# Optimization experiments

Hardware: AMD Instinct MI355X
Metric: run time of the kernel (lower is better)

## Reference

```python
import jax, jax.numpy as jnp
import numpy as np

B, T, NQ, NG = 8, 64, 900, 24
COST_CLS, COST_L1, COST_GIOU = 1.0, 5.0, 2.0
ALPHA, GAMMA = 0.25, 2.0


def _to_xyxy(b):
    cx, cy, w, h = b[..., 0], b[..., 1], b[..., 2], b[..., 3]
    return cx - w / 2, cy - h / 2, cx + w / 2, cy + h / 2


def _giou(a, b):
    # a, b: broadcastable (..., 4) boxes in cxcywh
    ax1, ay1, ax2, ay2 = _to_xyxy(a)
    bx1, by1, bx2, by2 = _to_xyxy(b)
    ix1 = jnp.maximum(ax1, bx1); iy1 = jnp.maximum(ay1, by1)
    ix2 = jnp.minimum(ax2, bx2); iy2 = jnp.minimum(ay2, by2)
    inter = jnp.clip(ix2 - ix1, 0) * jnp.clip(iy2 - iy1, 0)
    area_a = (ax2 - ax1) * (ay2 - ay1)
    area_b = (bx2 - bx1) * (by2 - by1)
    union = area_a + area_b - inter
    iou = inter / jnp.maximum(union, 1e-6)
    ex1 = jnp.minimum(ax1, bx1); ey1 = jnp.minimum(ay1, by1)
    ex2 = jnp.maximum(ax2, bx2); ey2 = jnp.maximum(ay2, by2)
    enc = (ex2 - ex1) * (ey2 - ey1)
    return iou - (enc - union) / jnp.maximum(enc, 1e-6)


def _cost(bboxes, scores, gt):
    # fully batched cost-matrix build across all B*T frames: (B,T,Nq,Ng)
    prob = jax.nn.sigmoid(scores)[..., 0]
    c_cls = -prob[..., None]
    c_l1 = jnp.abs(bboxes[:, :, :, None, :] - gt[:, :, None, :, :]).sum(-1)
    g = _giou(bboxes[:, :, :, None, :], gt[:, :, None, :, :])
    return COST_CLS * c_cls + COST_L1 * c_l1 - COST_GIOU * g


def _lsa(cost):
    # exact rectangular Hungarian (Jonker-Volgenant / e-maxx potentials).
    # cost: (n, m) with n <= m. Returns the column assigned to each row.
    n, m = cost.shape
    u = np.zeros(n + 1); v = np.zeros(m + 1)
    p = np.zeros(m + 1, dtype=np.int64)
    way = np.zeros(m + 1, dtype=np.int64)
    for i in range(1, n + 1):
        p[0] = i; j0 = 0
        minv = np.full(m + 1, np.inf)
        used = np.zeros(m + 1, dtype=bool)
        while True:
            used[j0] = True
            i0 = p[j0]
            jidx = np.nonzero(~used[1:])[0] + 1
            cur = cost[i0 - 1, jidx - 1] - u[i0] - v[jidx]
            better = cur < minv[jidx]
            minv[jidx] = np.where(better, cur, minv[jidx])
            way[jidx[better]] = j0
            k = jidx[np.argmin(minv[jidx])]
            delta = minv[k]
            u[p[used]] += delta
            v[used] -= delta
            minv[~used] -= delta
            j0 = k
            if p[j0] == 0:
                break
        while j0:
            j1 = way[j0]; p[j0] = p[j1]; j0 = j1
    col = np.zeros(n, dtype=np.int64)
    for j in range(1, m + 1):
        if p[j] > 0:
            col[p[j] - 1] = j - 1
    return col


def _match_all(bboxes, scores, gt):
    # mirrors the torch module's host-side scipy linear_sum_assignment per frame
    C = np.asarray(_cost(bboxes, scores, gt)).reshape(B * T, NQ, NG)
    match = np.stack([_lsa(C[f].T) for f in range(B * T)])  # query idx per GT
    return jnp.asarray(match.reshape(B, T, NG).astype(np.int32))


def _loss(bboxes, scores, gt, match):
    # focal classification loss over all queries
    tgt = jnp.minimum(jax.nn.one_hot(match, NQ, dtype=bboxes.dtype).sum(2), 1.0)[..., None]
    x = scores
    ce = tgt * jax.nn.softplus(-x) + (1.0 - tgt) * jax.nn.softplus(x)
    prob = jax.nn.sigmoid(x)
    pt = prob * tgt + (1.0 - prob) * (1.0 - tgt)
    fw = (ALPHA * tgt + (1.0 - ALPHA) * (1.0 - tgt)) * (1.0 - pt) ** GAMMA
    loss_cls = jnp.mean(fw * ce, axis=(2, 3))  # per-frame mean -> (B,T)
    idx = jnp.broadcast_to(match[..., None], (B, T, NG, 4))
    mp = jnp.take_along_axis(bboxes, idx, axis=2)  # (B,T,Ng,4)
    loss_l1 = jnp.mean(jnp.abs(mp - gt), axis=(2, 3))
    loss_g = jnp.mean(1.0 - _giou(mp, gt), axis=2)
    total = jnp.sum(loss_cls + 5.0 * loss_l1 + 2.0 * loss_g) / (B * T)
    return total.reshape(1)


def setup_inputs() -> dict:
    key = jax.random.key(0)
    k1, k2, k3 = jax.random.split(key, 3)
    return {
        "bboxes": jax.random.uniform(k1, (B, T, NQ, 4), dtype=jnp.float32),
        "scores": jax.random.normal(k2, (B, T, NQ, 1), dtype=jnp.float32),
        "gt_boxes": jax.random.uniform(k3, (B, T, NG, 4), dtype=jnp.float32),
    }


def reference(bboxes, scores, gt_boxes):
    match = _match_all(bboxes, scores, gt_boxes)
    return _loss(bboxes, scores, gt_boxes, match)
```

## Files before the change

kernel.cpp:

```cpp
#include <hip/hip_runtime.h>
#include <math.h>
#include <float.h>

#define NF 512
#define NQ 900
#define NG 24
#define NW 4
#define NCPL 4

#define ALPHA 0.25f

__device__ __forceinline__ unsigned monof(float f) {
    unsigned u = __float_as_uint(f);
    return (u & 0x80000000u) ? ~u : (u | 0x80000000u);
}
__device__ __forceinline__ float unmonof(unsigned m) {
    return (m & 0x80000000u) ? __uint_as_float(m ^ 0x80000000u)
                             : __uint_as_float(~m);
}

__device__ __forceinline__ float softplusf_(float x) {
    return fmaxf(x, 0.0f) + log1pf(expf(-fabsf(x)));
}

template <int CTRL, int RMASK>
__device__ __forceinline__ unsigned long long dpp_min_step(unsigned long long key) {
    const unsigned olo = (unsigned)__builtin_amdgcn_update_dpp(
        -1, (int)(unsigned)key, CTRL, RMASK, 0xf, false);
    const unsigned ohi = (unsigned)__builtin_amdgcn_update_dpp(
        -1, (int)(unsigned)(key >> 32), CTRL, RMASK, 0xf, false);
    const unsigned long long o = ((unsigned long long)ohi << 32) | olo;
    return (o < key) ? o : key;
}

__global__ __launch_bounds__(256) void fused_kernel(
        const float* __restrict__ bboxes,
        const float* __restrict__ scores,
        const float* __restrict__ gt,
        float* __restrict__ out)
{
    const int f = blockIdx.x;
    const int tid = threadIdx.x;
    const int lane = tid & 63;
    const int wid = tid >> 6;

    __shared__ float4 sgt[NG];
    __shared__ float u_[NG + 1];
    __shared__ int p[NQ + 1];
    __shared__ int way[NQ + 1];
    __shared__ unsigned long long swv[2][NW];
    __shared__ float lsum[NW];

    if (tid < NG) sgt[tid] = reinterpret_cast<const float4*>(gt + (size_t)f * NG * 4)[tid];

    float4 myb[NCPL];
    float myx[NCPL], ccls[NCPL], ccls2[NCPL];
    float ax1[NCPL], ay1[NCPL], ax2[NCPL], ay2[NCPL], areaA[NCPL];
    #pragma unroll
    for (int k = 0; k < NCPL; ++k) {
        const int c = tid + (k << 8);
        if (c < NQ) {
            float4 a = reinterpret_cast<const float4*>(bboxes + (size_t)f * NQ * 4)[c];
            myb[k] = a;
            float x = scores[(size_t)f * NQ + c];
            myx[k] = x;
            ccls[k] = -1.0f / (1.0f + expf(-x));
            ccls2[k] = ccls[k];
            ax1[k] = a.x - 0.5f * a.z; ay1[k] = a.y - 0.5f * a.w;
            ax2[k] = a.x + 0.5f * a.z; ay2[k] = a.y + 0.5f * a.w;
            areaA[k] = (ax2[k] - ax1[k]) * (ay2[k] - ay1[k]);
        }
    }
    for (int j = tid; j <= NQ; j += 256) p[j] = 0;
    if (tid <= NG) u_[tid] = 0.0f;
    __syncthreads();

    for (int i = 1; i <= NG; ++i) {
        float dist[NCPL], sjoin[NCPL];
        #pragma unroll
        for (int k = 0; k < NCPL; ++k) { dist[k] = INFINITY; sjoin[k] = 0.0f; }
        unsigned usedmask = 0;
        if (tid == 0) p[0] = i;

        int j0 = 0; float S = 0.0f; int it = 0;
        while (true) {
            const int i0 = (j0 == 0) ? i : p[j0];
            const float ui0 = u_[i0];
            const float4 g4 = sgt[i0 - 1];
            const float bx1 = g4.x - 0.5f * g4.z, by1 = g4.y - 0.5f * g4.w;
            const float bx2 = g4.x + 0.5f * g4.z, by2 = g4.y + 0.5f * g4.w;
            const float areaB = (bx2 - bx1) * (by2 - by1);
            const float base = S - ui0;

            if (j0 >= 1) {
                const int c0 = j0 - 1;
                if ((c0 & 255) == tid) { const int kk = c0 >> 8; usedmask |= 1u << kk; sjoin[kk] = S; }
            }

            float bestv = INFINITY; int bestj = 0x7fffffff;
            #pragma unroll
            for (int k = 0; k < NCPL; ++k) {
                const int c = tid + (k << 8);
                if (c < NQ && !((usedmask >> k) & 1u)) {
                    const float4 a = myb[k];
                    const float l1 = fabsf(a.x - g4.x) + fabsf(a.y - g4.y)
                                   + fabsf(a.z - g4.z) + fabsf(a.w - g4.w);
                    const float dx = fmaxf(fminf(ax2[k], bx2) - fmaxf(ax1[k], bx1), 0.0f);
                    const float dy = fmaxf(fminf(ay2[k], by2) - fmaxf(ay1[k], by1), 0.0f);
                    const float inter = dx * dy;
                    const float un = areaA[k] + areaB - inter;
                    const float ex = fmaxf(ax2[k], bx2) - fminf(ax1[k], bx1);
                    const float ey = fmaxf(ay2[k], by2) - fminf(ay1[k], by1);
                    const float enc = ex * ey;
                    const float unc = fmaxf(un, 1e-6f);
                    const float encc = fmaxf(enc, 1e-6f);
                    const float r = __builtin_amdgcn_rcpf(unc * encc);
                    const float gi = fmaf(-(enc - un), unc, inter * encc) * r;
                    const float cur = base + fmaf(5.0f, l1, ccls2[k]) - 2.0f * gi;
                    if (cur < dist[k]) { dist[k] = cur; way[c + 1] = j0; }
                    if (dist[k] < bestv) { bestv = dist[k]; bestj = c + 1; }
                }
            }
            unsigned long long bestkey =
                ((unsigned long long)monof(bestv) << 32) | (unsigned)bestj;
            bestkey = dpp_min_step<0x111, 0xf>(bestkey);
            bestkey = dpp_min_step<0x112, 0xf>(bestkey);
            bestkey = dpp_min_step<0x114, 0xf>(bestkey);
            bestkey = dpp_min_step<0x118, 0xf>(bestkey);
            bestkey = dpp_min_step<0x142, 0xa>(bestkey);
            bestkey = dpp_min_step<0x143, 0xc>(bestkey);
            const unsigned rlo = (unsigned)__builtin_amdgcn_readlane((int)(unsigned)bestkey, 63);
            const unsigned rhi = (unsigned)__builtin_amdgcn_readlane((int)(unsigned)(bestkey >> 32), 63);
            const unsigned long long wkey = ((unsigned long long)rhi << 32) | rlo;

            const int buf = it & 1;
            if (lane == 0) swv[buf][wid] = wkey;
            __syncthreads();
            unsigned long long m = swv[buf][0];
            #pragma unroll
            for (int w = 1; w < NW; ++w) { const unsigned long long o = swv[buf][w]; if (o < m) m = o; }
            const int j1 = (int)(m & 0xffffffffu);
            S = unmonof((unsigned)(m >> 32));
            j0 = j1; ++it;
            if (p[j1] == 0) break;
        }

        const float Send = S;
        if (tid == 0) u_[i] += Send;
        #pragma unroll
        for (int k = 0; k < NCPL; ++k) {
            if ((usedmask >> k) & 1u) {
                const int c = tid + (k << 8);
                const float dd = Send - sjoin[k];
                u_[p[c + 1]] += dd;
                ccls2[k] += dd;
            }
        }
        __syncthreads();
        if (tid == 0) { int jj = j0; while (jj) { const int jn = way[jj]; p[jj] = p[jn]; jj = jn; } }
        __syncthreads();
    }

    float val = 0.0f;
    #pragma unroll
    for (int k = 0; k < NCPL; ++k) {
        const int c = tid + (k << 8);
        if (c < NQ) {
            const float x = myx[k];
            const int pj = p[c + 1];
            const float t = (pj > 0) ? 1.0f : 0.0f;
            const float ce = t * softplusf_(-x) + (1.0f - t) * softplusf_(x);
            const float prob = -ccls[k];
            const float pt = prob * t + (1.0f - prob) * (1.0f - t);
            const float om = 1.0f - pt;
            const float fw = (ALPHA * t + (1.0f - ALPHA) * (1.0f - t)) * om * om;
            val += (fw * ce) * (1.0f / (float)NQ);
            if (pj > 0) {
                const float4 g4 = sgt[pj - 1];
                const float4 a = myb[k];
                const float l1 = fabsf(a.x - g4.x) + fabsf(a.y - g4.y)
                               + fabsf(a.z - g4.z) + fabsf(a.w - g4.w);
                const float bx1 = g4.x - 0.5f * g4.z, by1 = g4.y - 0.5f * g4.w;
                const float bx2 = g4.x + 0.5f * g4.z, by2 = g4.y + 0.5f * g4.w;
                const float ix1 = fmaxf(ax1[k], bx1), iy1 = fmaxf(ay1[k], by1);
                const float ix2 = fminf(ax2[k], bx2), iy2 = fminf(ay2[k], by2);
                const float inter = fmaxf(ix2 - ix1, 0.0f) * fmaxf(iy2 - iy1, 0.0f);
                const float areaB = (bx2 - bx1) * (by2 - by1);
                const float un = areaA[k] + areaB - inter;
                const float iou = inter / fmaxf(un, 1e-6f);
                const float ex1 = fminf(ax1[k], bx1), ey1 = fminf(ay1[k], by1);
                const float ex2 = fmaxf(ax2[k], bx2), ey2 = fmaxf(ay2[k], by2);
                const float enc = (ex2 - ex1) * (ey2 - ey1);
                const float gi = iou - (enc - un) / fmaxf(enc, 1e-6f);
                val += (5.0f / 96.0f) * l1 + (2.0f / 24.0f) * (1.0f - gi);
            }
        }
    }
    #pragma unroll
    for (int off = 32; off >= 1; off >>= 1) val += __shfl_xor(val, off);
    if (lane == 0) lsum[wid] = val;
    __syncthreads();
    if (tid == 0) {
        const float tot = lsum[0] + lsum[1] + lsum[2] + lsum[3];
        atomicAdd(out, tot * (1.0f / (float)NF));
    }
}

extern "C" void kernel_launch(void* const* d_in, const int* in_sizes, int n_in,
                              void* d_out, int out_size, void* d_ws, size_t ws_size,
                              hipStream_t stream) {
    const float* bboxes = (const float*)d_in[0];
    const float* scores = (const float*)d_in[1];
    const float* gt     = (const float*)d_in[2];
    float* out = (float*)d_out;

    hipLaunchKernelGGL(fused_kernel, dim3(NF), dim3(256), 0, stream, bboxes, scores, gt, out);
}
```

Measured before the change: 101.9 us.

## Add greedy row-min initialization to skip Hungarian augmentations for uncontested rows

Before the Hungarian loop, each row's minimum-cost column is computed in parallel and used as the initial dual u. Rows whose argmin column is not yet taken are assigned directly, and only the conflicting rows run the full Dijkstra-style augmentation. This aims to cut the number of sequential, barrier-heavy augmenting searches, which dominate per-frame latency. It adds one parallel pass over the cost matrix plus a serial fixup on a single thread. Exactness relies on the row-min duals staying feasible with v equal to zero, and the later v and loss code must handle columns matched without a search.

```diff
diff --git a/kernel.cpp b/kernel.cpp
--- a/kernel.cpp
+++ b/kernel.cpp
@@ -31,6 +31,15 @@
         -1, (int)(unsigned)(key >> 32), CTRL, RMASK, 0xf, false);
     const unsigned long long o = ((unsigned long long)ohi << 32) | olo;
     return (o < key) ? o : key;
+}
+__device__ __forceinline__ unsigned long long dpp_wave_min(unsigned long long k) {
+    k = dpp_min_step<0x111, 0xf>(k);
+    k = dpp_min_step<0x112, 0xf>(k);
+    k = dpp_min_step<0x114, 0xf>(k);
+    k = dpp_min_step<0x118, 0xf>(k);
+    k = dpp_min_step<0x142, 0xa>(k);
+    k = dpp_min_step<0x143, 0xc>(k);
+    return k;
 }
 
 __global__ __launch_bounds__(256) void fused_kernel(
@@ -49,6 +58,8 @@
     __shared__ int p[NQ + 1];
     __shared__ int way[NQ + 1];
     __shared__ unsigned long long swv[2][NW];
+    __shared__ unsigned long long swr[NG][NW];
+    __shared__ unsigned sfree;
     __shared__ float lsum[NW];
 
     if (tid < NG) sgt[tid] = reinterpret_cast<const float4*>(gt + (size_t)f * NG * 4)[tid];
@@ -75,7 +86,58 @@
     if (tid <= NG) u_[tid] = 0.0f;
     __syncthreads();
 
+    for (int r = 0; r < NG; ++r) {
+        const float4 g4 = sgt[r];
+        const float bx1 = g4.x - 0.5f * g4.z, by1 = g4.y - 0.5f * g4.w;
+        const float bx2 = g4.x + 0.5f * g4.z, by2 = g4.y + 0.5f * g4.w;
+        const float areaB = (bx2 - bx1) * (by2 - by1);
+        float bestv = INFINITY; int bestj = 0x7fffffff;
+        #pragma unroll
+        for (int k = 0; k < NCPL; ++k) {
+            const int c = tid + (k << 8);
+            if (c < NQ) {
+                const float4 a = myb[k];
+                const float l1 = fabsf(a.x - g4.x) + fabsf(a.y - g4.y)
+                               + fabsf(a.z - g4.z) + fabsf(a.w - g4.w);
+                const float dx = fmaxf(fminf(ax2[k], bx2) - fmaxf(ax1[k], bx1), 0.0f);
+                const float dy = fmaxf(fminf(ay2[k], by2) - fmaxf(ay1[k], by1), 0.0f);
+                const float inter = dx * dy;
+                const float un = areaA[k] + areaB - inter;
+                const float ex = fmaxf(ax2[k], bx2) - fminf(ax1[k], bx1);
+                const float ey = fmaxf(ay2[k], by2) - fminf(ay1[k], by1);
+                const float enc = ex * ey;
+                const float unc = fmaxf(un, 1e-6f);
+                const float encc = fmaxf(enc, 1e-6f);
+                const float rr = __builtin_amdgcn_rcpf(unc * encc);
+                const float gi = fmaf(-(enc - un), unc, inter * encc) * rr;
+                const float cost = fmaf(5.0f, l1, ccls[k]) - 2.0f * gi;
+                if (cost < bestv) { bestv = cost; bestj = c + 1; }
+            }
+        }
+        unsigned long long key =
+            ((unsigned long long)monof(bestv) << 32) | (unsigned)bestj;
+        key = dpp_wave_min(key);
+        if (lane == 63) swr[r][wid] = key;
+    }
+    __syncthreads();
+    if (tid == 0) {
+        unsigned freemask = 0;
+        for (int r = 0; r < NG; ++r) {
+            unsigned long long m = swr[r][0];
+            #pragma unroll
+            for (int w = 1; w < NW; ++w) { const unsigned long long o = swr[r][w]; if (o < m) m = o; }
+            const int col = (int)(m & 0xffffffffu);
+            u_[r + 1] = unmonof((unsigned)(m >> 32));
+            if (p[col] == 0) p[col] = r + 1;
+            else freemask |= 1u << r;
+        }
+        sfree = freemask;
+    }
+    __syncthreads();
+    const unsigned freemask = sfree;
+
     for (int i = 1; i <= NG; ++i) {
+        if (!((freemask >> (i - 1)) & 1u)) continue;
         float dist[NCPL], sjoin[NCPL];
         #pragma unroll
         for (int k = 0; k < NCPL; ++k) { dist[k] = INFINITY; sjoin[k] = 0.0f; }
@@ -123,12 +185,7 @@
             }
             unsigned long long bestkey =
                 ((unsigned long long)monof(bestv) << 32) | (unsigned)bestj;
-            bestkey = dpp_min_step<0x111, 0xf>(bestkey);
-            bestkey = dpp_min_step<0x112, 0xf>(bestkey);
-            bestkey = dpp_min_step<0x114, 0xf>(bestkey);
-            bestkey = dpp_min_step<0x118, 0xf>(bestkey);
-            bestkey = dpp_min_step<0x142, 0xa>(bestkey);
-            bestkey = dpp_min_step<0x143, 0xc>(bestkey);
+            bestkey = dpp_wave_min(bestkey);
             const unsigned rlo = (unsigned)__builtin_amdgcn_readlane((int)(unsigned)bestkey, 63);
             const unsigned rhi = (unsigned)__builtin_amdgcn_readlane((int)(unsigned)(bestkey >> 32), 63);
             const unsigned long long wkey = ((unsigned long long)rhi << 32) | rlo;
```

New measurement: 93.29 us. 1.09x faster.
